# Performance work log

Hardware: AMD Instinct MI355X
Metric: run time of the kernel (lower is better)

Reference implementation:

```python
import jax, jax.numpy as jnp
import numpy as np

BN_EPS = 1e-5


def maxpool2(x):
    # 2x2 max pool, stride 2: (B,C,H,W) -> (B,C,H//2,W//2)
    B, C, H, W = x.shape
    return x.reshape(B, C, H // 2, 2, W // 2, 2).max(axis=(3, 5))


def setup_inputs() -> dict:
    key = jax.random.key(0)
    ks = jax.random.split(key, 6)
    B, C, H, W = 4, 64, 96, 96   # in_dim = 64
    K, OD = 64, 64               # key_dim, out_dim
    sc = lambda fan: 1.0 / np.sqrt(fan)
    return {
        "c2": jax.random.normal(ks[0], (B, C, H, W), jnp.float32),
        "x": jax.random.normal(ks[1], (B, C, H, W), jnp.float32),
        # edge_att: Conv2d(2C->OD, 1x1, no bias) -> BN -> ReLU -> Conv2d(OD->1, 1x1) -> Sigmoid
        "w_ea1": jax.random.normal(ks[2], (OD, 2 * C), jnp.float32) * sc(2 * C),
        "bn_w": jnp.ones((OD,), jnp.float32),
        "bn_b": jnp.zeros((OD,), jnp.float32),
        "bn_m": jnp.zeros((OD,), jnp.float32),
        "bn_v": jnp.ones((OD,), jnp.float32),
        "w_ea2": jax.random.normal(ks[3], (1, OD), jnp.float32) * sc(OD),
        "b_ea2": jnp.zeros((1,), jnp.float32),
        # query_conv (shared for query AND key in the original forward)
        "w_q": jax.random.normal(ks[4], (K, C), jnp.float32) * sc(C),
        "b_q": jnp.zeros((K,), jnp.float32),
        "gamma": jnp.full((1,), 0.5, jnp.float32),
    }


def reference(c2, x, w_ea1, bn_w, bn_b, bn_m, bn_v, w_ea2, b_ea2, w_q, b_q, gamma):
    xp = maxpool2(x)        # (B,C,Hp,Wp)
    c2p = maxpool2(c2)
    B, C, H, W = x.shape
    Hp, Wp = xp.shape[2], xp.shape[3]

    # edge attention gate on pooled features -> (B,1,Hp,Wp)
    cat = jnp.concatenate([c2p, xp], axis=1)                       # (B,2C,Hp,Wp)
    h = jnp.einsum('oc,bchw->bohw', w_ea1, cat)
    bn_scale = (bn_w / jnp.sqrt(bn_v + BN_EPS))[None, :, None, None]
    h = jax.nn.relu((h - bn_m[None, :, None, None]) * bn_scale + bn_b[None, :, None, None])
    ea = jax.nn.sigmoid(jnp.einsum('oc,bchw->bohw', w_ea2, h) + b_ea2[None, :, None, None])

    # query at full res, key at pooled res (SAME conv weights, as in the source)
    q = jnp.einsum('kc,bchw->bkhw', w_q, x) + b_q[None, :, None, None]    # (B,K,H,W)
    k = jnp.einsum('kc,bchw->bkhw', w_q, xp) + b_q[None, :, None, None]   # (B,K,Hp,Wp)

    pq = q.reshape(B, -1, H * W)        # (B,K,N)
    pk = k.reshape(B, -1, Hp * Wp)      # (B,K,M)
    energy = jnp.einsum('bkn,bkm->bnm', pq, pk)                    # (B,N,M)
    attn = jax.nn.softmax(energy * ea.reshape(B, 1, Hp * Wp), axis=-1)

    v = xp.reshape(B, C, Hp * Wp)                                   # (B,C,M)
    out = jnp.einsum('bcm,bnm->bcn', v, attn).reshape(B, C, H, W)
    return gamma[0] * out + x
```

## Files before the change

kernel.cpp:

```cpp
#include <hip/hip_runtime.h>
#include <stdint.h>

#define B_ 4
#define C_ 64
#define H_ 96
#define W_ 96
#define HP_ 48
#define WP_ 48
#define N_ (H_*W_)
#define M_ (HP_*WP_)
#define KD_ 64
#define OD_ 64
#define BN_EPS 1e-5f
#define LOG2E 1.4426950408889634f
#define SHIFT2 28.853900817779268f
#define QT_ 48
#define QI_ (QT_/16)
#define QB_ (N_/QT_)
#define KVB_ 128
#define NT2_ (M_/KVB_)
#define KBUF_ 16384
#define BUF_ 32768
#define EAOFF_ 65536

typedef __bf16 bf16_t;
typedef bf16_t bf16x8 __attribute__((ext_vector_type(8)));
typedef bf16_t bf16x4 __attribute__((ext_vector_type(4)));
typedef float f32x4 __attribute__((ext_vector_type(4)));
typedef short short4v __attribute__((ext_vector_type(4)));
typedef short short8v __attribute__((ext_vector_type(8)));

static __device__ __forceinline__ unsigned short f2bf(float f) {
    unsigned int u = __builtin_bit_cast(unsigned int, f);
    u += 0x7fffu + ((u >> 16) & 1u);
    return (unsigned short)(u >> 16);
}

static __device__ __forceinline__ void gl_lds16(const unsigned short* g, unsigned short* l) {
#if __has_builtin(__builtin_amdgcn_global_load_lds)
    __builtin_amdgcn_global_load_lds(
        (const __attribute__((address_space(1))) unsigned int*)(const void*)g,
        (__attribute__((address_space(3))) unsigned int*)(void*)l, 16, 0, 0);
#endif
}

static __device__ __forceinline__ void setprio1() {
#if __has_builtin(__builtin_amdgcn_s_setprio)
    __builtin_amdgcn_s_setprio(1);
#endif
}
static __device__ __forceinline__ void setprio0() {
#if __has_builtin(__builtin_amdgcn_s_setprio)
    __builtin_amdgcn_s_setprio(0);
#endif
}
static __device__ __forceinline__ void schedbar0() {
#if __has_builtin(__builtin_amdgcn_sched_barrier)
    __builtin_amdgcn_sched_barrier(0);
#endif
}
static __device__ __forceinline__ void rawbar() {
#if __has_builtin(__builtin_amdgcn_s_barrier)
    __builtin_amdgcn_s_barrier();
#else
    __syncthreads();
#endif
}

__global__ __launch_bounds__(256) void prep_kernel(
    const float* __restrict__ x, const float* __restrict__ c2,
    const float* __restrict__ wq, const float* __restrict__ bq,
    const float* __restrict__ w1, const float* __restrict__ bnw, const float* __restrict__ bnb,
    const float* __restrict__ bnm, const float* __restrict__ bnv,
    const float* __restrict__ w2, const float* __restrict__ b2,
    unsigned short* __restrict__ kb, unsigned short* __restrict__ vb, float* __restrict__ ea) {

    __shared__ float lw1[OD_*2*C_];
    __shared__ float lwq[KD_*C_];
    __shared__ float xs[C_*33];
    __shared__ float c2s[C_*33];
    __shared__ float red[8][32];

    int tid = threadIdx.x;
    int b = blockIdx.x / 72;
    int m0 = (blockIdx.x % 72) * 32;

    for (int i = tid; i < OD_*2*C_; i += 256) lw1[i] = w1[i];
    for (int i = tid; i < KD_*C_; i += 256) lwq[i] = wq[i];
    for (int j = tid; j < 2048; j += 256) {
        int c = j >> 5, p = j & 31;
        int m = m0 + p;
        int hp = m / WP_, wp = m % WP_;
        size_t base = ((size_t)(b*C_ + c)*H_ + 2*hp)*W_ + 2*wp;
        const float* px = x + base;
        float mx = fmaxf(fmaxf(px[0], px[1]), fmaxf(px[W_], px[W_+1]));
        xs[c*33 + p] = mx;
        vb[(size_t)(b*C_ + c)*M_ + m] = f2bf(mx);
        const float* pc = c2 + base;
        c2s[c*33 + p] = fmaxf(fmaxf(pc[0], pc[1]), fmaxf(pc[W_], pc[W_+1]));
    }
    __syncthreads();

    int ml = tid & 31, oz = tid >> 5;
    int m = m0 + ml;

    float h[8] = {0,0,0,0,0,0,0,0};
    for (int c = 0; c < C_; c += 4) {
        float x0 = xs[c*33+ml], x1 = xs[(c+1)*33+ml], x2 = xs[(c+2)*33+ml], x3 = xs[(c+3)*33+ml];
        #pragma unroll
        for (int oi = 0; oi < 8; oi++) {
            const float4 wv = *(const float4*)&lwq[(oz*8 + oi)*C_ + c];
            h[oi] = fmaf(wv.x, x0, fmaf(wv.y, x1, fmaf(wv.z, x2, fmaf(wv.w, x3, h[oi]))));
        }
    }
    unsigned short tmp[8];
    #pragma unroll
    for (int oi = 0; oi < 8; oi++) tmp[oi] = f2bf(h[oi] + bq[oz*8 + oi]);
    *(uint4*)&kb[((size_t)b*M_ + m)*KD_ + oz*8] = *(const uint4*)tmp;

    float g[8] = {0,0,0,0,0,0,0,0};
    for (int c = 0; c < 2*C_; c += 4) {
        const float* srcb = (c < C_) ? &c2s[c*33] : &xs[(c - C_)*33];
        float x0 = srcb[ml], x1 = srcb[33+ml], x2 = srcb[66+ml], x3 = srcb[99+ml];
        #pragma unroll
        for (int oi = 0; oi < 8; oi++) {
            const float4 wv = *(const float4*)&lw1[(oz*8 + oi)*(2*C_) + c];
            g[oi] = fmaf(wv.x, x0, fmaf(wv.y, x1, fmaf(wv.z, x2, fmaf(wv.w, x3, g[oi]))));
        }
    }
    float z = 0.f;
    #pragma unroll
    for (int oi = 0; oi < 8; oi++) {
        int o = oz*8 + oi;
        float sc = bnw[o] * rsqrtf(bnv[o] + BN_EPS);
        float t = (g[oi] - bnm[o]) * sc + bnb[o];
        z += w2[o] * fmaxf(t, 0.f);
    }
    red[oz][ml] = z;
    __syncthreads();
    if (oz == 0) {
        float s = b2[0];
        #pragma unroll
        for (int i = 0; i < 8; i++) s += red[i][ml];
        ea[(size_t)b*M_ + m] = LOG2E / (1.f + __builtin_amdgcn_exp2f(-s * LOG2E));
    }
}

__global__ __launch_bounds__(256, 2) void attn_kernel(
    const float* __restrict__ wq, const float* __restrict__ bq,
    const unsigned short* __restrict__ kb, const unsigned short* __restrict__ vb,
    const float* __restrict__ ea, const float* __restrict__ x,
    const float* __restrict__ gamma_p, float* __restrict__ out) {

    __shared__ __align__(16) char smem[74752];

    int tid = threadIdx.x;
    int wave = tid >> 6, lane = tid & 63, quad = lane >> 4, l16 = lane & 15;
    int blk = blockIdx.x;
    int b = (blk & 7) >> 1;
    int n_base = ((blk & 1) * (QB_/2) + (blk >> 3)) * QT_;
    int xsw = l16 & 7;

    unsigned short* qlds = (unsigned short*)(smem + EAOFF_);
    {
        const float* xb = x + (size_t)b*C_*N_ + n_base;
        bf16x8 wh0, wh1, wl0, wl1;
        {
            float w8[8];
            unsigned short hs[8], ls[8];
            const float* wp0 = wq + (size_t)(wave*16 + l16)*C_ + quad*8;
            *(float4*)&w8[0] = *(const float4*)wp0;
            *(float4*)&w8[4] = *(const float4*)(wp0 + 4);
            #pragma unroll
            for (int j = 0; j < 8; j++) {
                hs[j] = f2bf(w8[j]);
                float hf = __builtin_bit_cast(float, (unsigned int)hs[j] << 16);
                ls[j] = f2bf(w8[j] - hf);
            }
            wh0 = __builtin_bit_cast(bf16x8, *(const uint4*)hs);
            wl0 = __builtin_bit_cast(bf16x8, *(const uint4*)ls);
            const float* wp1 = wp0 + 32;
            *(float4*)&w8[0] = *(const float4*)wp1;
            *(float4*)&w8[4] = *(const float4*)(wp1 + 4);
            #pragma unroll
            for (int j = 0; j < 8; j++) {
                hs[j] = f2bf(w8[j]);
                float hf = __builtin_bit_cast(float, (unsigned int)hs[j] << 16);
                ls[j] = f2bf(w8[j] - hf);
            }
            wh1 = __builtin_bit_cast(bf16x8, *(const uint4*)hs);
            wl1 = __builtin_bit_cast(bf16x8, *(const uint4*)ls);
        }
        float4 bq4 = *(const float4*)(bq + wave*16 + quad*4);

        f32x4 qacc[3];
        #pragma unroll
        for (int t = 0; t < 3; t++) qacc[t] = (f32x4){0.f,0.f,0.f,0.f};

        #pragma unroll
        for (int t = 0; t < 3; t++) {
            #pragma unroll
            for (int h = 0; h < 2; h++) {
                float v8[8];
                #pragma unroll
                for (int j = 0; j < 8; j++)
                    v8[j] = xb[(size_t)(h*32 + quad*8 + j)*N_ + t*16 + l16];
                unsigned short hs[8], ls[8];
                #pragma unroll
                for (int j = 0; j < 8; j++) {
                    hs[j] = f2bf(v8[j]);
                    float hf = __builtin_bit_cast(float, (unsigned int)hs[j] << 16);
                    ls[j] = f2bf(v8[j] - hf);
                }
                bf16x8 xh = __builtin_bit_cast(bf16x8, *(const uint4*)hs);
                bf16x8 xl = __builtin_bit_cast(bf16x8, *(const uint4*)ls);
                bf16x8 wh = h ? wh1 : wh0;
                bf16x8 wl = h ? wl1 : wl0;
#if __has_builtin(__builtin_amdgcn_mfma_f32_16x16x32_bf16)
                qacc[t] = __builtin_amdgcn_mfma_f32_16x16x32_bf16(wh, xh, qacc[t], 0, 0, 0);
                qacc[t] = __builtin_amdgcn_mfma_f32_16x16x32_bf16(wl, xh, qacc[t], 0, 0, 0);
                qacc[t] = __builtin_amdgcn_mfma_f32_16x16x32_bf16(wh, xl, qacc[t], 0, 0, 0);
#endif
            }
        }
        #pragma unroll
        for (int t = 0; t < 3; t++) {
            unsigned short q4[4];
            q4[0] = f2bf(qacc[t][0] + bq4.x);
            q4[1] = f2bf(qacc[t][1] + bq4.y);
            q4[2] = f2bf(qacc[t][2] + bq4.z);
            q4[3] = f2bf(qacc[t][3] + bq4.w);
            int n_abs = t*16 + l16;
            int kc = wave*2 + (quad >> 1);
            *(uint2*)&qlds[n_abs*64 + ((kc ^ (n_abs & 7)) << 3) + (quad & 1)*4] =
                *(const uint2*)q4;
        }
    }
    asm volatile("s_waitcnt lgkmcnt(0)" ::: "memory");
    __syncthreads();

    bf16x8 qf[QI_][2];
    #pragma unroll
    for (int qi = 0; qi < QI_; qi++) {
        const unsigned short* qp = qlds + (qi*16 + l16)*64;
        qf[qi][0] = __builtin_bit_cast(bf16x8, *(const uint4*)(qp + ((quad     ^ xsw) << 3)));
        qf[qi][1] = __builtin_bit_cast(bf16x8, *(const uint4*)(qp + (((quad+4) ^ xsw) << 3)));
    }
    asm volatile("s_waitcnt lgkmcnt(0)" ::: "memory");
    __syncthreads();

    f32x4 o2[QI_][4];
    f32x4 lacc[QI_];
    #pragma unroll
    for (int qi = 0; qi < QI_; qi++) {
        lacc[qi] = (f32x4){0.f,0.f,0.f,0.f};
        #pragma unroll
        for (int ct = 0; ct < 4; ct++) o2[qi][ct] = (f32x4){0.f,0.f,0.f,0.f};
    }
    const unsigned short ones_u[8] = {0x3F80,0x3F80,0x3F80,0x3F80,0x3F80,0x3F80,0x3F80,0x3F80};
    bf16x8 ones8 = __builtin_bit_cast(bf16x8, *(const uint4*)ones_u);

    const unsigned short* kbB = kb + (size_t)b*M_*KD_;
    const unsigned short* vbB = vb + (size_t)b*C_*M_;
    const float* eaB = ea + (size_t)b*M_;

    int r8  = tid >> 3;
    int mloc = (((r8 & 15) >> 2) << 3) + ((r8 >> 4) << 2) + (r8 & 3);
    int kcs = ((tid & 7) ^ (r8 & 7)) << 3;
    int c16 = tid >> 4;
    int vcs = ((tid & 15) ^ (c16 & 7)) << 3;

    auto STAGE = [&](int mb, char* buf) {
        unsigned short* kd = (unsigned short*)buf;
        unsigned short* vd = (unsigned short*)(buf + KBUF_);
        gl_lds16(kbB + (size_t)(mb +  0 + mloc)*KD_ + kcs, kd + 0*2048 + tid*8);
        gl_lds16(kbB + (size_t)(mb + 32 + mloc)*KD_ + kcs, kd + 1*2048 + tid*8);
        gl_lds16(kbB + (size_t)(mb + 64 + mloc)*KD_ + kcs, kd + 2*2048 + tid*8);
        gl_lds16(kbB + (size_t)(mb + 96 + mloc)*KD_ + kcs, kd + 3*2048 + tid*8);
        gl_lds16(vbB + (size_t)( 0 + c16)*M_ + mb + vcs, vd + 0*2048 + tid*8);
        gl_lds16(vbB + (size_t)(16 + c16)*M_ + mb + vcs, vd + 1*2048 + tid*8);
        gl_lds16(vbB + (size_t)(32 + c16)*M_ + mb + vcs, vd + 2*2048 + tid*8);
        gl_lds16(vbB + (size_t)(48 + c16)*M_ + mb + vcs, vd + 3*2048 + tid*8);
    };

    {
        const f32x4* eaV = (const f32x4*)eaB;
        f32x4* eaL = (f32x4*)(smem + EAOFF_);
        for (int i = tid; i < M_/4; i += 256) eaL[i] = eaV[i];
    }
    asm volatile("s_waitcnt lgkmcnt(0)" ::: "memory");
    __syncthreads();
    STAGE(0,    smem);
    STAGE(128,  smem + BUF_);
    asm volatile("s_waitcnt vmcnt(8)" ::: "memory");
    rawbar();
    asm volatile("" ::: "memory");

    const float* lds_ea = (const float*)(smem + EAOFF_);

    int kOffA0 = (wave*32 + l16)*64 + ((quad       ^ xsw) << 3);
    int kOffA1 = (wave*32 + l16)*64 + (((quad + 4) ^ xsw) << 3);
    int kOffB0 = kOffA0 + 16*64;
    int kOffB1 = kOffA1 + 16*64;
    int vch    = ((wave*4 + quad) ^ xsw) << 3;
    int eaIdx  = wave*32 + quad*8;

    struct FragSet {
        bf16x8 kfA0, kfA1, kfB0, kfB1;
        bf16x8 va0, va1, va2, va3;
        f32x4 eA, eB;
    };
    struct StSet { f32x4 sA[QI_]; f32x4 sB[QI_]; };
    FragSet fA, fB;
    StSet sX, sY;

    {
        unsigned short* kc = (unsigned short*)smem;
        unsigned short* vc = (unsigned short*)(smem + KBUF_);
        fA.eA  = *(const f32x4*)&lds_ea[0*KVB_ + eaIdx];
        fA.eB  = *(const f32x4*)&lds_ea[0*KVB_ + eaIdx + 4];
        fA.kfA0 = __builtin_bit_cast(bf16x8, *(const uint4*)(kc + kOffA0));
        fA.kfA1 = __builtin_bit_cast(bf16x8, *(const uint4*)(kc + kOffA1));
        fA.kfB0 = __builtin_bit_cast(bf16x8, *(const uint4*)(kc + kOffB0));
        fA.kfB1 = __builtin_bit_cast(bf16x8, *(const uint4*)(kc + kOffB1));
        fA.va0 = __builtin_bit_cast(bf16x8, *(const uint4*)(vc + (0*16 + l16)*KVB_ + vch));
        fA.va1 = __builtin_bit_cast(bf16x8, *(const uint4*)(vc + (1*16 + l16)*KVB_ + vch));
        fA.va2 = __builtin_bit_cast(bf16x8, *(const uint4*)(vc + (2*16 + l16)*KVB_ + vch));
        fA.va3 = __builtin_bit_cast(bf16x8, *(const uint4*)(vc + (3*16 + l16)*KVB_ + vch));
    }
    asm volatile("s_waitcnt lgkmcnt(0)" ::: "memory");
    schedbar0();
    #pragma unroll
    for (int qi = 0; qi < QI_; qi++) {
        f32x4 zA = (f32x4){0.f,0.f,0.f,0.f};
        zA = __builtin_amdgcn_mfma_f32_16x16x32_bf16(fA.kfA0, qf[qi][0], zA, 0, 0, 0);
        zA = __builtin_amdgcn_mfma_f32_16x16x32_bf16(fA.kfA1, qf[qi][1], zA, 0, 0, 0);
        sX.sA[qi] = zA;
        f32x4 zB = (f32x4){0.f,0.f,0.f,0.f};
        zB = __builtin_amdgcn_mfma_f32_16x16x32_bf16(fA.kfB0, qf[qi][0], zB, 0, 0, 0);
        zB = __builtin_amdgcn_mfma_f32_16x16x32_bf16(fA.kfB1, qf[qi][1], zB, 0, 0, 0);
        sX.sB[qi] = zB;
    }

#define ATTN_STEP(T_, CUR, NXT, SCUR, SNXT)                                            \
    {                                                                                  \
        const int t_ = (T_);                                                           \
        if (t_ < NT2_ - 1) {                                                           \
            asm volatile("s_waitcnt vmcnt(0)" ::: "memory");   \
            schedbar0();                                                               \
            rawbar();                    \
            asm volatile("" ::: "memory");                                             \
            schedbar0();                                                               \
            if (t_ + 2 < NT2_) { STAGE((t_ + 2)*KVB_, smem + (t_ & 1)*BUF_); }         \
            unsigned short* kc_ = (unsigned short*)(smem + ((t_ + 1) & 1)*BUF_);       \
            unsigned short* vc_ = (unsigned short*)(smem + ((t_ + 1) & 1)*BUF_ + KBUF_); \
            NXT.eA  = *(const f32x4*)&lds_ea[(t_ + 1)*KVB_ + eaIdx];                   \
            NXT.eB  = *(const f32x4*)&lds_ea[(t_ + 1)*KVB_ + eaIdx + 4];               \
            NXT.kfA0 = __builtin_bit_cast(bf16x8, *(const uint4*)(kc_ + kOffA0));      \
            NXT.kfA1 = __builtin_bit_cast(bf16x8, *(const uint4*)(kc_ + kOffA1));      \
            NXT.kfB0 = __builtin_bit_cast(bf16x8, *(const uint4*)(kc_ + kOffB0));      \
            NXT.kfB1 = __builtin_bit_cast(bf16x8, *(const uint4*)(kc_ + kOffB1));      \
            NXT.va0 = __builtin_bit_cast(bf16x8, *(const uint4*)(vc_ + (0*16 + l16)*KVB_ + vch)); \
            NXT.va1 = __builtin_bit_cast(bf16x8, *(const uint4*)(vc_ + (1*16 + l16)*KVB_ + vch)); \
            NXT.va2 = __builtin_bit_cast(bf16x8, *(const uint4*)(vc_ + (2*16 + l16)*KVB_ + vch)); \
            NXT.va3 = __builtin_bit_cast(bf16x8, *(const uint4*)(vc_ + (3*16 + l16)*KVB_ + vch)); \
            schedbar0();                                                               \
        }                                                                              \
                      \
        bf16x8 pk[QI_];                                                                \
        _Pragma("unroll")                                                              \
        for (int qi = 0; qi < QI_; qi++) {                                             \
            f32x4 pA, pB;                                                              \
            pA[0] = __builtin_amdgcn_exp2f(fmaf(SCUR.sA[qi][0], CUR.eA[0], -SHIFT2));  \
            pA[1] = __builtin_amdgcn_exp2f(fmaf(SCUR.sA[qi][1], CUR.eA[1], -SHIFT2));  \
            pA[2] = __builtin_amdgcn_exp2f(fmaf(SCUR.sA[qi][2], CUR.eA[2], -SHIFT2));  \
            pA[3] = __builtin_amdgcn_exp2f(fmaf(SCUR.sA[qi][3], CUR.eA[3], -SHIFT2));  \
            pB[0] = __builtin_amdgcn_exp2f(fmaf(SCUR.sB[qi][0], CUR.eB[0], -SHIFT2));  \
            pB[1] = __builtin_amdgcn_exp2f(fmaf(SCUR.sB[qi][1], CUR.eB[1], -SHIFT2));  \
            pB[2] = __builtin_amdgcn_exp2f(fmaf(SCUR.sB[qi][2], CUR.eB[2], -SHIFT2));  \
            pB[3] = __builtin_amdgcn_exp2f(fmaf(SCUR.sB[qi][3], CUR.eB[3], -SHIFT2));  \
            short4v pa = __builtin_bit_cast(short4v, __builtin_convertvector(pA, bf16x4)); \
            short4v pb = __builtin_bit_cast(short4v, __builtin_convertvector(pB, bf16x4)); \
            short8v p8 = __builtin_shufflevector(pa, pb, 0, 1, 2, 3, 4, 5, 6, 7);      \
            pk[qi] = __builtin_bit_cast(bf16x8, p8);                                   \
        }                                                                              \
        setprio1();                                                                    \
        _Pragma("unroll")                                                              \
        for (int qi = 0; qi < QI_; qi++) {                                             \
            o2[qi][0] = __builtin_amdgcn_mfma_f32_16x16x32_bf16(CUR.va0, pk[qi], o2[qi][0], 0, 0, 0); \
            o2[qi][1] = __builtin_amdgcn_mfma_f32_16x16x32_bf16(CUR.va1, pk[qi], o2[qi][1], 0, 0, 0); \
            o2[qi][2] = __builtin_amdgcn_mfma_f32_16x16x32_bf16(CUR.va2, pk[qi], o2[qi][2], 0, 0, 0); \
            o2[qi][3] = __builtin_amdgcn_mfma_f32_16x16x32_bf16(CUR.va3, pk[qi], o2[qi][3], 0, 0, 0); \
            lacc[qi]  = __builtin_amdgcn_mfma_f32_16x16x32_bf16(ones8,   pk[qi], lacc[qi], 0, 0, 0); \
        }                                                                              \
        setprio0();                                                                    \
            \
        if (t_ < NT2_ - 1) {                                                           \
            asm volatile("s_waitcnt lgkmcnt(0)" ::: "memory");   \
            schedbar0();                                \
            setprio1();                                                                \
            _Pragma("unroll")                                                          \
            for (int qi = 0; qi < QI_; qi++) {                                         \
                f32x4 zA = (f32x4){0.f,0.f,0.f,0.f};                                   \
                zA = __builtin_amdgcn_mfma_f32_16x16x32_bf16(NXT.kfA0, qf[qi][0], zA, 0, 0, 0); \
                zA = __builtin_amdgcn_mfma_f32_16x16x32_bf16(NXT.kfA1, qf[qi][1], zA, 0, 0, 0); \
                SNXT.sA[qi] = zA;                                                      \
                f32x4 zB = (f32x4){0.f,0.f,0.f,0.f};                                   \
                zB = __builtin_amdgcn_mfma_f32_16x16x32_bf16(NXT.kfB0, qf[qi][0], zB, 0, 0, 0); \
                zB = __builtin_amdgcn_mfma_f32_16x16x32_bf16(NXT.kfB1, qf[qi][1], zB, 0, 0, 0); \
                SNXT.sB[qi] = zB;                                                      \
            }                                                                          \
            setprio0();                                                                \
        }                                                                              \
    }

    for (int t = 0; t < NT2_; t += 2) {
        ATTN_STEP(t,     fA, fB, sX, sY);
        ATTN_STEP(t + 1, fB, fA, sY, sX);
    }
#undef ATTN_STEP

    __syncthreads();

    float* o_red0 = (float*)smem;
    float* o_red1 = o_red0 + QT_*68;
    float* l_red  = o_red1 + QT_*68;

    if (lane < 16) {
        #pragma unroll
        for (int qi = 0; qi < QI_; qi++) l_red[wave*QT_ + qi*16 + l16] = lacc[qi][0];
    }
    if (wave < 2) {
        float* od = (wave == 0) ? o_red0 : o_red1;
        #pragma unroll
        for (int qi = 0; qi < QI_; qi++)
            #pragma unroll
            for (int ct = 0; ct < 4; ct++)
                *(f32x4*)&od[(qi*16 + l16)*68 + ct*16 + quad*4] = o2[qi][ct];
    }
    __syncthreads();
    if (wave >= 2) {
        float* od = (wave == 2) ? o_red0 : o_red1;
        #pragma unroll
        for (int qi = 0; qi < QI_; qi++)
            #pragma unroll
            for (int ct = 0; ct < 4; ct++) {
                f32x4* p = (f32x4*)&od[(qi*16 + l16)*68 + ct*16 + quad*4];
                *p += o2[qi][ct];
            }
    }
    __syncthreads();
    if (tid < QT_) {
        float s = (l_red[tid] + l_red[QT_ + tid]) + (l_red[2*QT_ + tid] + l_red[3*QT_ + tid]);
        l_red[tid] = 1.f / s;
    }
    __syncthreads();

    float gmm = gamma_p[0];
    int c = tid >> 2, q4 = tid & 3;
    const float* xrow = x + ((size_t)b*C_ + c)*N_ + n_base;
    float* orow = out + ((size_t)b*C_ + c)*N_ + n_base;
    #pragma unroll
    for (int i = 0; i < QI_; i++) {
        int q0 = q4*4 + i*16;
        float4 xv = *(const float4*)(xrow + q0);
        float4 ov;
        float v0 = (o_red0[(q0+0)*68 + c] + o_red1[(q0+0)*68 + c]) * l_red[q0+0];
        float v1 = (o_red0[(q0+1)*68 + c] + o_red1[(q0+1)*68 + c]) * l_red[q0+1];
        float v2 = (o_red0[(q0+2)*68 + c] + o_red1[(q0+2)*68 + c]) * l_red[q0+2];
        float v3 = (o_red0[(q0+3)*68 + c] + o_red1[(q0+3)*68 + c]) * l_red[q0+3];
        ov.x = fmaf(gmm, v0, xv.x);
        ov.y = fmaf(gmm, v1, xv.y);
        ov.z = fmaf(gmm, v2, xv.z);
        ov.w = fmaf(gmm, v3, xv.w);
        *(float4*)(orow + q0) = ov;
    }
}

extern "C" void kernel_launch(void* const* d_in, const int* in_sizes, int n_in,
                              void* d_out, int out_size, void* d_ws, size_t ws_size,
                              hipStream_t stream) {
    const float* c2    = (const float*)d_in[0];
    const float* x     = (const float*)d_in[1];
    const float* w_ea1 = (const float*)d_in[2];
    const float* bn_w  = (const float*)d_in[3];
    const float* bn_b  = (const float*)d_in[4];
    const float* bn_m  = (const float*)d_in[5];
    const float* bn_v  = (const float*)d_in[6];
    const float* w_ea2 = (const float*)d_in[7];
    const float* b_ea2 = (const float*)d_in[8];
    const float* w_q   = (const float*)d_in[9];
    const float* b_q   = (const float*)d_in[10];
    const float* gamma = (const float*)d_in[11];
    float* out = (float*)d_out;

    char* ws = (char*)d_ws;
    float* ea            = (float*)(ws + 0);
    unsigned short* kb   = (unsigned short*)(ws + 36864);
    unsigned short* vb   = (unsigned short*)(ws + 1216512);

    prep_kernel<<<dim3((B_*M_)/32), dim3(256), 0, stream>>>(x, c2, w_q, b_q,
        w_ea1, bn_w, bn_b, bn_m, bn_v, w_ea2, b_ea2, kb, vb, ea);
    attn_kernel<<<dim3(B_*QB_), dim3(256), 0, stream>>>(w_q, b_q, kb, vb, ea, x, gamma, out);
}
```

Measured before the change: 149.6 us.

## Fold edge-attention gate into keys and drop fixed softmax shift

The prep kernel now computes the sigmoid edge gate first and multiplies each key vector by it (including the log2e factor) before storing bf16 keys. The attention kernel no longer stages the gate array into LDS or loads per-tile gate fragments, and the exponent becomes a plain exp2 of the score without the fused multiply and constant shift. This removes LDS traffic, registers and per-element FMAs from the hot loop and shrinks shared memory. In exchange, the pre-scaled keys are rounded to bf16, and dropping the constant shift relies on scores staying within exp2's fp32 range.

```diff
diff --git a/kernel.cpp b/kernel.cpp
--- a/kernel.cpp
+++ b/kernel.cpp
@@ -13,7 +13,6 @@
 #define OD_ 64
 #define BN_EPS 1e-5f
 #define LOG2E 1.4426950408889634f
-#define SHIFT2 28.853900817779268f
 #define QT_ 48
 #define QI_ (QT_/16)
 #define QB_ (N_/QT_)
@@ -21,7 +20,6 @@
 #define NT2_ (M_/KVB_)
 #define KBUF_ 16384
 #define BUF_ 32768
-#define EAOFF_ 65536
 
 typedef __bf16 bf16_t;
 typedef bf16_t bf16x8 __attribute__((ext_vector_type(8)));
@@ -73,13 +71,14 @@
     const float* __restrict__ w1, const float* __restrict__ bnw, const float* __restrict__ bnb,
     const float* __restrict__ bnm, const float* __restrict__ bnv,
     const float* __restrict__ w2, const float* __restrict__ b2,
-    unsigned short* __restrict__ kb, unsigned short* __restrict__ vb, float* __restrict__ ea) {
+    unsigned short* __restrict__ kb, unsigned short* __restrict__ vb) {
 
     __shared__ float lw1[OD_*2*C_];
     __shared__ float lwq[KD_*C_];
     __shared__ float xs[C_*33];
     __shared__ float c2s[C_*33];
     __shared__ float red[8][32];
+    __shared__ float eaf[32];
 
     int tid = threadIdx.x;
     int b = blockIdx.x / 72;
@@ -104,20 +103,6 @@
     int ml = tid & 31, oz = tid >> 5;
     int m = m0 + ml;
 
-    float h[8] = {0,0,0,0,0,0,0,0};
-    for (int c = 0; c < C_; c += 4) {
-        float x0 = xs[c*33+ml], x1 = xs[(c+1)*33+ml], x2 = xs[(c+2)*33+ml], x3 = xs[(c+3)*33+ml];
-        #pragma unroll
-        for (int oi = 0; oi < 8; oi++) {
-            const float4 wv = *(const float4*)&lwq[(oz*8 + oi)*C_ + c];
-            h[oi] = fmaf(wv.x, x0, fmaf(wv.y, x1, fmaf(wv.z, x2, fmaf(wv.w, x3, h[oi]))));
-        }
-    }
-    unsigned short tmp[8];
-    #pragma unroll
-    for (int oi = 0; oi < 8; oi++) tmp[oi] = f2bf(h[oi] + bq[oz*8 + oi]);
-    *(uint4*)&kb[((size_t)b*M_ + m)*KD_ + oz*8] = *(const uint4*)tmp;
-
     float g[8] = {0,0,0,0,0,0,0,0};
     for (int c = 0; c < 2*C_; c += 4) {
         const float* srcb = (c < C_) ? &c2s[c*33] : &xs[(c - C_)*33];
@@ -142,17 +127,32 @@
         float s = b2[0];
         #pragma unroll
         for (int i = 0; i < 8; i++) s += red[i][ml];
-        ea[(size_t)b*M_ + m] = LOG2E / (1.f + __builtin_amdgcn_exp2f(-s * LOG2E));
-    }
+        eaf[ml] = LOG2E / (1.f + __builtin_amdgcn_exp2f(-s * LOG2E));
+    }
+    __syncthreads();
+
+    float h[8] = {0,0,0,0,0,0,0,0};
+    for (int c = 0; c < C_; c += 4) {
+        float x0 = xs[c*33+ml], x1 = xs[(c+1)*33+ml], x2 = xs[(c+2)*33+ml], x3 = xs[(c+3)*33+ml];
+        #pragma unroll
+        for (int oi = 0; oi < 8; oi++) {
+            const float4 wv = *(const float4*)&lwq[(oz*8 + oi)*C_ + c];
+            h[oi] = fmaf(wv.x, x0, fmaf(wv.y, x1, fmaf(wv.z, x2, fmaf(wv.w, x3, h[oi]))));
+        }
+    }
+    float fac = eaf[ml];
+    unsigned short tmp[8];
+    #pragma unroll
+    for (int oi = 0; oi < 8; oi++) tmp[oi] = f2bf((h[oi] + bq[oz*8 + oi]) * fac);
+    *(uint4*)&kb[((size_t)b*M_ + m)*KD_ + oz*8] = *(const uint4*)tmp;
 }
 
 __global__ __launch_bounds__(256, 2) void attn_kernel(
     const float* __restrict__ wq, const float* __restrict__ bq,
     const unsigned short* __restrict__ kb, const unsigned short* __restrict__ vb,
-    const float* __restrict__ ea, const float* __restrict__ x,
-    const float* __restrict__ gamma_p, float* __restrict__ out) {
-
-    __shared__ __align__(16) char smem[74752];
+    const float* __restrict__ x, const float* __restrict__ gamma_p, float* __restrict__ out) {
+
+    __shared__ __align__(16) char smem[65536];
 
     int tid = threadIdx.x;
     int wave = tid >> 6, lane = tid & 63, quad = lane >> 4, l16 = lane & 15;
@@ -161,7 +161,7 @@
     int n_base = ((blk & 1) * (QB_/2) + (blk >> 3)) * QT_;
     int xsw = l16 & 7;
 
-    unsigned short* qlds = (unsigned short*)(smem + EAOFF_);
+    unsigned short* qlds = (unsigned short*)smem;
     {
         const float* xb = x + (size_t)b*C_*N_ + n_base;
         bf16x8 wh0, wh1, wl0, wl1;
@@ -262,7 +262,6 @@
 
     const unsigned short* kbB = kb + (size_t)b*M_*KD_;
     const unsigned short* vbB = vb + (size_t)b*C_*M_;
-    const float* eaB = ea + (size_t)b*M_;
 
     int r8  = tid >> 3;
     int mloc = (((r8 & 15) >> 2) << 3) + ((r8 >> 4) << 2) + (r8 & 3);
@@ -283,32 +282,21 @@
         gl_lds16(vbB + (size_t)(48 + c16)*M_ + mb + vcs, vd + 3*2048 + tid*8);
     };
 
-    {
-        const f32x4* eaV = (const f32x4*)eaB;
-        f32x4* eaL = (f32x4*)(smem + EAOFF_);
-        for (int i = tid; i < M_/4; i += 256) eaL[i] = eaV[i];
-    }
-    asm volatile("s_waitcnt lgkmcnt(0)" ::: "memory");
-    __syncthreads();
     STAGE(0,    smem);
     STAGE(128,  smem + BUF_);
     asm volatile("s_waitcnt vmcnt(8)" ::: "memory");
     rawbar();
     asm volatile("" ::: "memory");
 
-    const float* lds_ea = (const float*)(smem + EAOFF_);
-
     int kOffA0 = (wave*32 + l16)*64 + ((quad       ^ xsw) << 3);
     int kOffA1 = (wave*32 + l16)*64 + (((quad + 4) ^ xsw) << 3);
     int kOffB0 = kOffA0 + 16*64;
     int kOffB1 = kOffA1 + 16*64;
     int vch    = ((wave*4 + quad) ^ xsw) << 3;
-    int eaIdx  = wave*32 + quad*8;
 
     struct FragSet {
         bf16x8 kfA0, kfA1, kfB0, kfB1;
         bf16x8 va0, va1, va2, va3;
-        f32x4 eA, eB;
     };
     struct StSet { f32x4 sA[QI_]; f32x4 sB[QI_]; };
     FragSet fA, fB;
@@ -317,8 +305,6 @@
     {
         unsigned short* kc = (unsigned short*)smem;
         unsigned short* vc = (unsigned short*)(smem + KBUF_);
-        fA.eA  = *(const f32x4*)&lds_ea[0*KVB_ + eaIdx];
-        fA.eB  = *(const f32x4*)&lds_ea[0*KVB_ + eaIdx + 4];
         fA.kfA0 = __builtin_bit_cast(bf16x8, *(const uint4*)(kc + kOffA0));
         fA.kfA1 = __builtin_bit_cast(bf16x8, *(const uint4*)(kc + kOffA1));
         fA.kfB0 = __builtin_bit_cast(bf16x8, *(const uint4*)(kc + kOffB0));
@@ -354,8 +340,6 @@
             if (t_ + 2 < NT2_) { STAGE((t_ + 2)*KVB_, smem + (t_ & 1)*BUF_); }         \
             unsigned short* kc_ = (unsigned short*)(smem + ((t_ + 1) & 1)*BUF_);       \
             unsigned short* vc_ = (unsigned short*)(smem + ((t_ + 1) & 1)*BUF_ + KBUF_); \
-            NXT.eA  = *(const f32x4*)&lds_ea[(t_ + 1)*KVB_ + eaIdx];                   \
-            NXT.eB  = *(const f32x4*)&lds_ea[(t_ + 1)*KVB_ + eaIdx + 4];               \
             NXT.kfA0 = __builtin_bit_cast(bf16x8, *(const uint4*)(kc_ + kOffA0));      \
             NXT.kfA1 = __builtin_bit_cast(bf16x8, *(const uint4*)(kc_ + kOffA1));      \
             NXT.kfB0 = __builtin_bit_cast(bf16x8, *(const uint4*)(kc_ + kOffB0));      \
@@ -371,14 +355,14 @@
         _Pragma("unroll")                                                              \
         for (int qi = 0; qi < QI_; qi++) {                                             \
             f32x4 pA, pB;                                                              \
-            pA[0] = __builtin_amdgcn_exp2f(fmaf(SCUR.sA[qi][0], CUR.eA[0], -SHIFT2));  \
-            pA[1] = __builtin_amdgcn_exp2f(fmaf(SCUR.sA[qi][1], CUR.eA[1], -SHIFT2));  \
-            pA[2] = __builtin_amdgcn_exp2f(fmaf(SCUR.sA[qi][2], CUR.eA[2], -SHIFT2));  \
-            pA[3] = __builtin_amdgcn_exp2f(fmaf(SCUR.sA[qi][3], CUR.eA[3], -SHIFT2));  \
-            pB[0] = __builtin_amdgcn_exp2f(fmaf(SCUR.sB[qi][0], CUR.eB[0], -SHIFT2));  \
-            pB[1] = __builtin_amdgcn_exp2f(fmaf(SCUR.sB[qi][1], CUR.eB[1], -SHIFT2));  \
-            pB[2] = __builtin_amdgcn_exp2f(fmaf(SCUR.sB[qi][2], CUR.eB[2], -SHIFT2));  \
-            pB[3] = __builtin_amdgcn_exp2f(fmaf(SCUR.sB[qi][3], CUR.eB[3], -SHIFT2));  \
+            pA[0] = __builtin_amdgcn_exp2f(SCUR.sA[qi][0]);                            \
+            pA[1] = __builtin_amdgcn_exp2f(SCUR.sA[qi][1]);                            \
+            pA[2] = __builtin_amdgcn_exp2f(SCUR.sA[qi][2]);                            \
+            pA[3] = __builtin_amdgcn_exp2f(SCUR.sA[qi][3]);                            \
+            pB[0] = __builtin_amdgcn_exp2f(SCUR.sB[qi][0]);                            \
+            pB[1] = __builtin_amdgcn_exp2f(SCUR.sB[qi][1]);                            \
+            pB[2] = __builtin_amdgcn_exp2f(SCUR.sB[qi][2]);                            \
+            pB[3] = __builtin_amdgcn_exp2f(SCUR.sB[qi][3]);                            \
             short4v pa = __builtin_bit_cast(short4v, __builtin_convertvector(pA, bf16x4)); \
             short4v pb = __builtin_bit_cast(short4v, __builtin_convertvector(pB, bf16x4)); \
             short8v p8 = __builtin_shufflevector(pa, pb, 0, 1, 2, 3, 4, 5, 6, 7);      \
@@ -495,11 +479,10 @@
     float* out = (float*)d_out;
 
     char* ws = (char*)d_ws;
-    float* ea            = (float*)(ws + 0);
-    unsigned short* kb   = (unsigned short*)(ws + 36864);
-    unsigned short* vb   = (unsigned short*)(ws + 1216512);
+    unsigned short* kb   = (unsigned short*)(ws + 0);
+    unsigned short* vb   = (unsigned short*)(ws + 1179648);
 
     prep_kernel<<<dim3((B_*M_)/32), dim3(256), 0, stream>>>(x, c2, w_q, b_q,
-        w_ea1, bn_w, bn_b, bn_m, bn_v, w_ea2, b_ea2, kb, vb, ea);
-    attn_kernel<<<dim3(B_*QB_), dim3(256), 0, stream>>>(w_q, b_q, kb, vb, ea, x, gamma, out);
-}
+        w_ea1, bn_w, bn_b, bn_m, bn_v, w_ea2, b_ea2, kb, vb);
+    attn_kernel<<<dim3(B_*QB_), dim3(256), 0, stream>>>(w_q, b_q, kb, vb, x, gamma, out);
+}
```

After: 146.0 us. -2.4%, faster.
